# Kernel optimization log

Measured on AMD Instinct MI355X. Metric: run time of the kernel, lower is better.

## Reference

```python
import jax, jax.numpy as jnp
import numpy as np

B, S, D, H = 2, 2048, 1024, 16
HD = D // H  # head_dim = 64


def setup_inputs() -> dict:
    key = jax.random.key(0)
    ks = jax.random.split(key, 11)
    s = 0.02  # keep projections well-scaled
    return {
        "Q": jax.random.normal(ks[0], (B, S, D), jnp.float32),
        "K": jax.random.normal(ks[1], (B, S, D), jnp.float32),
        "V": jax.random.normal(ks[2], (B, S, D), jnp.float32),
        "Wq": jax.random.normal(ks[3], (D, D), jnp.float32) * s,
        "bq": jax.random.normal(ks[4], (D,), jnp.float32) * s,
        "Wk": jax.random.normal(ks[5], (D, D), jnp.float32) * s,
        "bk": jax.random.normal(ks[6], (D,), jnp.float32) * s,
        "Wv": jax.random.normal(ks[7], (D, D), jnp.float32) * s,
        "bv": jax.random.normal(ks[8], (D,), jnp.float32) * s,
        "Wo": jax.random.normal(ks[9], (D, D), jnp.float32) * s,
        "bo": jax.random.normal(ks[10], (D,), jnp.float32) * s,
    }


def reference(Q, K, V, Wq, bq, Wk, bk, Wv, bv, Wo, bo):
    b, s, d = Q.shape
    # projections (torch Linear: x @ W.T + b)
    q = (Q @ Wq.T + bq).reshape(b, s, H, HD).transpose(0, 2, 1, 3)  # [B,H,S,HD]
    k = (K @ Wk.T + bk).reshape(b, s, H, HD).transpose(0, 2, 1, 3)
    v = (V @ Wv.T + bv).reshape(b, s, H, HD).transpose(0, 2, 1, 3)
    # scaled dot-product scores: [B,H,S,S]
    scale = 1.0 / jnp.sqrt(jnp.asarray(HD, q.dtype))
    scores = jnp.einsum("bhqd,bhkd->bhqk", q, k) * scale
    # module's explicit max-subtract before softmax
    scores = scores - jnp.max(scores, axis=-1, keepdims=True)
    attn = jax.nn.softmax(scores, axis=-1)
    # dropout p=0.0 (eval) -> identity; renormalize-after-dropout kept verbatim
    attn = attn / jnp.sum(attn, axis=-1, keepdims=True)
    ctx = jnp.einsum("bhqk,bhkd->bhqd", attn, v)  # [B,H,S,HD]
    ctx = ctx.transpose(0, 2, 1, 3).reshape(b, s, d)
    out = ctx @ Wo.T + bo
    return out
```

## Files before the change

kernel.cpp:

```cpp
#include <hip/hip_runtime.h>

#define SS 2048
#define SD 1024
#define SH 16
#define SHD 64
#define MROWS 4096
#define LOG2E 1.44269504088896340736f

typedef __attribute__((ext_vector_type(8))) short short8;
typedef __attribute__((ext_vector_type(4))) short short4v;
typedef __attribute__((ext_vector_type(4))) float floatx4;
typedef __attribute__((ext_vector_type(4))) unsigned short ushort4v;
typedef unsigned short u16;
typedef unsigned int u32;

#define AS1 __attribute__((address_space(1)))
#define AS3 __attribute__((address_space(3)))

__device__ inline u16 f2bf(float v) {
  u32 x = __builtin_bit_cast(u32, v);
  x = x + 0x7fffu + ((x >> 16) & 1u);
  return (u16)(x >> 16);
}

__global__ __launch_bounds__(256) void cast_all(
    const float* __restrict__ q, const float* __restrict__ k,
    const float* __restrict__ v, const float* __restrict__ wq,
    const float* __restrict__ wk, const float* __restrict__ wv,
    const float* __restrict__ wo, u16* __restrict__ out) {
  int i = blockIdx.x * 256 + threadIdx.x;
  const float* src;
  int idx;
  if (i < 3145728) {
    int a = i >> 20;
    src = (a == 0) ? q : ((a == 1) ? k : v);
    idx = i & 1048575;
  } else {
    int j = i - 3145728;
    int a = j >> 18;
    src = (a == 0) ? wq : ((a == 1) ? wk : ((a == 2) ? wv : wo));
    idx = j & 262143;
  }
  float4 f = ((const float4*)src)[idx];
  ushort4v o;
  o[0] = f2bf(f.x); o[1] = f2bf(f.y); o[2] = f2bf(f.z); o[3] = f2bf(f.w);
  ((ushort4v*)out)[i] = o;
}

__global__ __launch_bounds__(256, 3) void gemm_bt(
    const u16* __restrict__ Aall, const u16* __restrict__ Wall,
    const float* __restrict__ b0, const float* __restrict__ b1,
    const float* __restrict__ b2, u16* __restrict__ outb,
    float* __restrict__ outf, int mode, float qscale) {
  __shared__ u16 smem[16384];
  u16* lds_a = smem;
  u16* lds_w = smem + 8192;
  int z = blockIdx.z;
  const u16* A = Aall + (size_t)z * (MROWS * (size_t)SD);
  const u16* W = Wall + (size_t)z * (SD * (size_t)SD);
  const float* bias = (z == 0) ? b0 : ((z == 1) ? b1 : b2);
  float scale = (mode == 0 && z == 0) ? qscale : 1.0f;

  int tid = threadIdx.x;
  int lane = tid & 63, wave = tid >> 6;
  int l16 = lane & 15, quad = lane >> 4;
  int wm = (wave >> 1) * 64, wn = (wave & 1) * 64;
  int tm = blockIdx.y * 128, tn = blockIdx.x * 128;

  floatx4 acc[4][4];
  floatx4 zf = {0.f, 0.f, 0.f, 0.f};
#pragma unroll
  for (int r = 0; r < 4; r++)
#pragma unroll
    for (int c = 0; c < 4; c++) acc[r][c] = zf;

  const u16* pa[4];
  const u16* pw[4];
#pragma unroll
  for (int q = 0; q < 4; q++) {
    int srow = q * 32 + wave * 8 + (lane >> 3);
    int scol = (((lane & 7) ^ ((lane >> 3) & 7)) << 3);
    pa[q] = A + (size_t)(tm + srow) * SD + scol;
    pw[q] = W + (size_t)(tn + srow) * SD + scol;
  }

  for (int k0 = 0; k0 < SD; k0 += 64) {
#pragma unroll
    for (int q = 0; q < 4; q++) {
      __builtin_amdgcn_global_load_lds((const AS1 void*)pa[q],
          (AS3 void*)(AS3 u16*)&lds_a[(q * 32 + wave * 8) * 64], 16, 0, 0);
      __builtin_amdgcn_global_load_lds((const AS1 void*)pw[q],
          (AS3 void*)(AS3 u16*)&lds_w[(q * 32 + wave * 8) * 64], 16, 0, 0);
      pa[q] += 64; pw[q] += 64;
    }
    __syncthreads();
    short8 af[4][2], wf[4][2];
#pragma unroll
    for (int r = 0; r < 4; r++)
#pragma unroll
      for (int kk = 0; kk < 2; kk++)
        af[r][kk] = *(short8*)&lds_a[(wm + r * 16 + l16) * 64 +
                                     (((kk * 4 + quad) ^ (l16 & 7)) << 3)];
#pragma unroll
    for (int c = 0; c < 4; c++)
#pragma unroll
      for (int kk = 0; kk < 2; kk++)
        wf[c][kk] = *(short8*)&lds_w[(wn + c * 16 + l16) * 64 +
                                     (((kk * 4 + quad) ^ (l16 & 7)) << 3)];
#pragma unroll
    for (int r = 0; r < 4; r++)
#pragma unroll
      for (int c = 0; c < 4; c++) {
        acc[r][c] = __builtin_amdgcn_mfma_f32_16x16x32_bf16(af[r][0], wf[c][0], acc[r][c], 0, 0, 0);
        acc[r][c] = __builtin_amdgcn_mfma_f32_16x16x32_bf16(af[r][1], wf[c][1], acc[r][c], 0, 0, 0);
      }
    __syncthreads();
  }

  if (mode == 0) {
    u16* ob = outb + (size_t)z * (MROWS * (size_t)SD);
    if (z < 2) {
      u16* LT = smem;
#pragma unroll
      for (int r = 0; r < 4; r++) {
#pragma unroll
        for (int c = 0; c < 4; c++) {
          int feat = wn + c * 16 + l16;
          float bv = bias[tn + feat];
#pragma unroll
          for (int g = 0; g < 4; g++) {
            int key = wm + r * 16 + quad * 4 + g;
            float val = (acc[r][c][g] + bv) * scale;
            LT[key * 128 + ((((feat >> 3) ^ (key & 7)) << 3) | (feat & 7))] = f2bf(val);
          }
        }
      }
      __syncthreads();
      int bb = tm >> 11;
      int kt0 = (tm & 2047) >> 6;
#pragma unroll
      for (int i = 0; i < 8; i++) {
        int id = wave * 8 + i;
        int kt_rel = id >> 4, hrel = (id >> 3) & 1, ct = (id >> 1) & 3, hh = id & 1;
        int key = kt_rel * 64 + ct * 16 + l16;
        int chunk = hrel * 8 + hh * 4 + quad;
        short8 vv = *(short8*)&LT[key * 128 + ((chunk ^ (l16 & 7)) << 3)];
        int h = (tn >> 6) + hrel;
        u16* dst = ob + (size_t)(bb * SH + h) * (SS * SHD) +
                   ((kt0 + kt_rel) * 8 + ct * 2 + hh) * 512 + lane * 8;
        *(short8*)dst = vv;
      }
    } else {
      int h = (tn + wn) >> 6;
      int bb = (tm + wm) >> 11;
      int kt = ((tm + wm) & 2047) >> 6;
      u16* vbase = ob + (size_t)(bb * SH + h) * (SS * SHD) + (size_t)kt * 4096 +
                   (l16 * 4 + quad) * 8;
#pragma unroll
      for (int c = 0; c < 4; c++) {
        int gn = tn + wn + c * 16 + l16;
        float bv = bias[gn];
#pragma unroll
        for (int rp = 0; rp < 2; rp++) {
          union { u16 u[8]; short8 s; } pk;
#pragma unroll
          for (int g = 0; g < 4; g++) {
            pk.u[g]     = f2bf(acc[2 * rp][c][g] + bv);
            pk.u[4 + g] = f2bf(acc[2 * rp + 1][c][g] + bv);
          }
          *(short8*)&vbase[(c * 2 + rp) * 512] = pk.s;
        }
      }
    }
  } else {
#pragma unroll
    for (int r = 0; r < 4; r++) {
#pragma unroll
      for (int c = 0; c < 4; c++) {
        int gn = tn + wn + c * 16 + l16;
        float bv = bias[gn];
#pragma unroll
        for (int g = 0; g < 4; g++) {
          int gm = tm + wm + r * 16 + quad * 4 + g;
          outf[(size_t)gm * SD + gn] = acc[r][c][g] + bv;
        }
      }
    }
  }
}

__global__ __launch_bounds__(128, 2) void attn(
    const u16* __restrict__ qb, const u16* __restrict__ kb,
    const u16* __restrict__ vfrag, u16* __restrict__ ctxb) {
  int lane = threadIdx.x & 63;
  int wave = threadIdx.x >> 6;
  int l16 = lane & 15, quad = lane >> 4;

  int raw = blockIdx.x;
  int xcd = raw & 7, slot = raw >> 3;
  int bh = xcd + 8 * (slot >> 5);
  int qt = slot & 31;
  int b = bh >> 4, h = bh & 15;
  int base = bh * (SS * SHD);
  int q0 = qt * 64;

  const u16* kp = kb + base + lane * 8;
  const u16* vp = vfrag + base + (l16 * 4 + quad) * 8;

  short8 qf[4][2];
#pragma unroll
  for (int t = 0; t < 4; t++)
#pragma unroll
    for (int hh = 0; hh < 2; hh++)
      qf[t][hh] = *(const short8*)&qb[base + (qt * 8 + t * 2 + hh) * 512 + lane * 8];

  floatx4 zf = {0.f, 0.f, 0.f, 0.f};
  floatx4 acc[4][4], accl[4];
#pragma unroll
  for (int t = 0; t < 4; t++) {
    accl[t] = zf;
#pragma unroll
    for (int c = 0; c < 4; c++) acc[t][c] = zf;
  }
  const short8 ones8 = {0x3F80, 0x3F80, 0x3F80, 0x3F80,
                        0x3F80, 0x3F80, 0x3F80, 0x3F80};

  int ktbase = wave * 16;
  short8 kf[4][2], vf[4][2];
  {
    const u16* p = kp + ktbase * 4096;
#pragma unroll
    for (int ct = 0; ct < 4; ct++)
#pragma unroll
      for (int hh = 0; hh < 2; hh++)
        kf[ct][hh] = *(const short8*)&p[(ct * 2 + hh) * 512];
    const u16* pv = vp + ktbase * 4096;
#pragma unroll
    for (int c = 0; c < 4; c++)
#pragma unroll
      for (int c2 = 0; c2 < 2; c2++)
        vf[c][c2] = *(const short8*)&pv[(c * 2 + c2) * 512];
  }

#pragma unroll 1
  for (int i = 0; i < 16; i++) {
    int nt = ktbase + ((i + 1) & 15);
    const u16* kpn = kp + nt * 4096;
    const u16* vpn = vp + nt * 4096;
#pragma unroll
    for (int c2 = 0; c2 < 2; c2++) {
      const int ct0 = 2 * c2, ct1 = 2 * c2 + 1;
      floatx4 se[4], so[4];
#pragma unroll
      for (int t = 0; t < 4; t++) {
        floatx4 zz = zf;
        zz = __builtin_amdgcn_mfma_f32_16x16x32_bf16(kf[ct0][0], qf[t][0], zz, 0, 0, 0);
        zz = __builtin_amdgcn_mfma_f32_16x16x32_bf16(kf[ct0][1], qf[t][1], zz, 0, 0, 0);
        se[t] = zz;
        floatx4 ww = zf;
        ww = __builtin_amdgcn_mfma_f32_16x16x32_bf16(kf[ct1][0], qf[t][0], ww, 0, 0, 0);
        ww = __builtin_amdgcn_mfma_f32_16x16x32_bf16(kf[ct1][1], qf[t][1], ww, 0, 0, 0);
        so[t] = ww;
      }
      kf[ct0][0] = *(const short8*)&kpn[(ct0 * 2 + 0) * 512];
      kf[ct0][1] = *(const short8*)&kpn[(ct0 * 2 + 1) * 512];
      kf[ct1][0] = *(const short8*)&kpn[(ct1 * 2 + 0) * 512];
      kf[ct1][1] = *(const short8*)&kpn[(ct1 * 2 + 1) * 512];
#pragma unroll
      for (int t = 0; t < 4; t++) {
        u32 e0 = __builtin_bit_cast(u32, __builtin_amdgcn_exp2f(se[t][0]));
        u32 e1 = __builtin_bit_cast(u32, __builtin_amdgcn_exp2f(se[t][1]));
        u32 e2 = __builtin_bit_cast(u32, __builtin_amdgcn_exp2f(se[t][2]));
        u32 e3 = __builtin_bit_cast(u32, __builtin_amdgcn_exp2f(se[t][3]));
        u32 o0 = __builtin_bit_cast(u32, __builtin_amdgcn_exp2f(so[t][0]));
        u32 o1 = __builtin_bit_cast(u32, __builtin_amdgcn_exp2f(so[t][1]));
        u32 o2 = __builtin_bit_cast(u32, __builtin_amdgcn_exp2f(so[t][2]));
        u32 o3 = __builtin_bit_cast(u32, __builtin_amdgcn_exp2f(so[t][3]));
        union { u32 u[4]; short8 s; } pa;
        pa.u[0] = __builtin_amdgcn_perm(e1, e0, 0x07060302);
        pa.u[1] = __builtin_amdgcn_perm(e3, e2, 0x07060302);
        pa.u[2] = __builtin_amdgcn_perm(o1, o0, 0x07060302);
        pa.u[3] = __builtin_amdgcn_perm(o3, o2, 0x07060302);
#pragma unroll
        for (int c = 0; c < 4; c++)
          acc[t][c] = __builtin_amdgcn_mfma_f32_16x16x32_bf16(pa.s, vf[c][c2], acc[t][c], 0, 0, 0);
        accl[t] = __builtin_amdgcn_mfma_f32_16x16x32_bf16(pa.s, ones8, accl[t], 0, 0, 0);
      }
#pragma unroll
      for (int c = 0; c < 4; c++)
        vf[c][c2] = *(const short8*)&vpn[(c * 2 + c2) * 512];
    }
  }

  __shared__ floatx4 red[2][64][11];
  int ow = 1 - wave;
#pragma unroll
  for (int t = 0; t < 4; t++) {
    if ((t >> 1) == ow) {
#pragma unroll
      for (int c = 0; c < 4; c++) red[ow][lane][(t & 1) * 5 + c] = acc[t][c];
      red[ow][lane][(t & 1) * 5 + 4] = accl[t];
    }
  }
  __syncthreads();
#pragma unroll
  for (int t = 0; t < 4; t++) {
    if ((t >> 1) == wave) {
#pragma unroll
      for (int c = 0; c < 4; c++) acc[t][c] += red[wave][lane][(t & 1) * 5 + c];
      accl[t] += red[wave][lane][(t & 1) * 5 + 4];
    }
  }

#pragma unroll
  for (int t = 0; t < 4; t++) {
    if ((t >> 1) == wave) {
#pragma unroll
      for (int g = 0; g < 4; g++) {
        float invg = 1.0f / accl[t][g];
        int qrow = q0 + t * 16 + quad * 4 + g;
#pragma unroll
        for (int c = 0; c < 4; c++) {
          int hd = c * 16 + l16;
          ctxb[(size_t)((b * SS + qrow) * SD + h * SHD + hd)] = f2bf(acc[t][c][g] * invg);
        }
      }
    }
  }
}

extern "C" void kernel_launch(void* const* d_in, const int* in_sizes, int n_in,
                              void* d_out, int out_size, void* d_ws, size_t ws_size,
                              hipStream_t stream) {
  const float* Q  = (const float*)d_in[0];
  const float* Kp = (const float*)d_in[1];
  const float* Vp = (const float*)d_in[2];
  const float* Wq = (const float*)d_in[3];
  const float* bq = (const float*)d_in[4];
  const float* Wk = (const float*)d_in[5];
  const float* bk = (const float*)d_in[6];
  const float* Wv = (const float*)d_in[7];
  const float* bv = (const float*)d_in[8];
  const float* Wo = (const float*)d_in[9];
  const float* bo = (const float*)d_in[10];

  u16* xb   = (u16*)d_ws;
  u16* wb   = xb + (size_t)3 * 4194304;
  u16* qkvb = wb + (size_t)4 * 1048576;
  u16* ctxb = qkvb + (size_t)3 * 4194304;
  float* out = (float*)d_out;

  cast_all<<<dim3(16384), dim3(256), 0, stream>>>(Q, Kp, Vp, Wq, Wk, Wv, Wo, xb);

  const float qscale = 0.125f * LOG2E;
  gemm_bt<<<dim3(8, 32, 3), dim3(256), 0, stream>>>(
      xb, wb, bq, bk, bv, qkvb, (float*)nullptr, 0, qscale);

  attn<<<dim3(1024), dim3(128), 0, stream>>>(
      qkvb, qkvb + (size_t)4194304, qkvb + (size_t)2 * 4194304, ctxb);

  gemm_bt<<<dim3(8, 32, 1), dim3(256), 0, stream>>>(
      ctxb, wb + (size_t)3 * 1048576, bo, bo, bo,
      (u16*)nullptr, out, 1, 1.0f);
}
```

Measured before the change: 206.7 us.

## Split attention key range across four waves with two-stage LDS reduction

The attention kernel now runs 256 threads (four waves) per block instead of two. Each wave handles eight key tiles instead of sixteen, and the partial accumulators are combined with a two-step butterfly reduction through shared memory. This is meant to raise per-block parallelism and latency hiding for the memory-bound K/V fragment loads. It adds an extra reduction stage, an extra barrier and more shared memory, and the launch bound of three blocks per CU may increase register pressure.

New measurement: 300.2 us. 45.2% more time.

```diff
diff --git a/kernel.cpp b/kernel.cpp
--- a/kernel.cpp
+++ b/kernel.cpp
@@ -8,7 +8,6 @@
 #define LOG2E 1.44269504088896340736f
 
 typedef __attribute__((ext_vector_type(8))) short short8;
-typedef __attribute__((ext_vector_type(4))) short short4v;
 typedef __attribute__((ext_vector_type(4))) float floatx4;
 typedef __attribute__((ext_vector_type(4))) unsigned short ushort4v;
 typedef unsigned short u16;
@@ -189,7 +188,7 @@
   }
 }
 
-__global__ __launch_bounds__(128, 2) void attn(
+__global__ __launch_bounds__(256, 3) void attn(
     const u16* __restrict__ qb, const u16* __restrict__ kb,
     const u16* __restrict__ vfrag, u16* __restrict__ ctxb) {
   int lane = threadIdx.x & 63;
@@ -225,7 +224,7 @@
   const short8 ones8 = {0x3F80, 0x3F80, 0x3F80, 0x3F80,
                         0x3F80, 0x3F80, 0x3F80, 0x3F80};
 
-  int ktbase = wave * 16;
+  int ktbase = wave * 8;
   short8 kf[4][2], vf[4][2];
   {
     const u16* p = kp + ktbase * 4096;
@@ -243,8 +242,8 @@
   }
 
 #pragma unroll 1
-  for (int i = 0; i < 16; i++) {
-    int nt = ktbase + ((i + 1) & 15);
+  for (int i = 0; i < 8; i++) {
+    int nt = ktbase + ((i + 1) & 7);
     const u16* kpn = kp + nt * 4096;
     const u16* vpn = vp + nt * 4096;
 #pragma unroll
@@ -292,29 +291,52 @@
     }
   }
 
-  __shared__ floatx4 red[2][64][11];
-  int ow = 1 - wave;
-#pragma unroll
-  for (int t = 0; t < 4; t++) {
-    if ((t >> 1) == ow) {
-#pragma unroll
-      for (int c = 0; c < 4; c++) red[ow][lane][(t & 1) * 5 + c] = acc[t][c];
-      red[ow][lane][(t & 1) * 5 + 4] = accl[t];
+  __shared__ floatx4 red[4][64][10];
+
+  int dest1 = wave ^ 1;
+#pragma unroll
+  for (int t = 0; t < 4; t++) {
+    if ((t >> 1) != (wave & 1)) {
+#pragma unroll
+      for (int c = 0; c < 4; c++) red[dest1][lane][(t & 1) * 5 + c] = acc[t][c];
+      red[dest1][lane][(t & 1) * 5 + 4] = accl[t];
     }
   }
   __syncthreads();
 #pragma unroll
   for (int t = 0; t < 4; t++) {
-    if ((t >> 1) == wave) {
+    if ((t >> 1) == (wave & 1)) {
 #pragma unroll
       for (int c = 0; c < 4; c++) acc[t][c] += red[wave][lane][(t & 1) * 5 + c];
       accl[t] += red[wave][lane][(t & 1) * 5 + 4];
     }
   }
-
-#pragma unroll
-  for (int t = 0; t < 4; t++) {
-    if ((t >> 1) == wave) {
+  __syncthreads();
+
+  int dest2 = wave ^ 2;
+  int t_pub = (wave & 1) * 2 + 1 - (wave >> 1);
+  int t_own = (wave & 1) * 2 + (wave >> 1);
+#pragma unroll
+  for (int t = 0; t < 4; t++) {
+    if (t == t_pub) {
+#pragma unroll
+      for (int c = 0; c < 4; c++) red[dest2][lane][c] = acc[t][c];
+      red[dest2][lane][4] = accl[t];
+    }
+  }
+  __syncthreads();
+#pragma unroll
+  for (int t = 0; t < 4; t++) {
+    if (t == t_own) {
+#pragma unroll
+      for (int c = 0; c < 4; c++) acc[t][c] += red[wave][lane][c];
+      accl[t] += red[wave][lane][4];
+    }
+  }
+
+#pragma unroll
+  for (int t = 0; t < 4; t++) {
+    if (t == t_own) {
 #pragma unroll
       for (int g = 0; g < 4; g++) {
         float invg = 1.0f / accl[t][g];
@@ -356,7 +378,7 @@
   gemm_bt<<<dim3(8, 32, 3), dim3(256), 0, stream>>>(
       xb, wb, bq, bk, bv, qkvb, (float*)nullptr, 0, qscale);
 
-  attn<<<dim3(1024), dim3(128), 0, stream>>>(
+  attn<<<dim3(1024), dim3(256), 0, stream>>>(
       qkvb, qkvb + (size_t)4194304, qkvb + (size_t)2 * 4194304, ctxb);
 
   gemm_bt<<<dim3(8, 32, 1), dim3(256), 0, stream>>>(
```
